# Optimization experiments

Hardware: AMD Instinct MI355X
Metric: run time of the kernel (lower is better)

The kernel has to match this reference:

```python
import jax, jax.numpy as jnp
import numpy as np

BATCH, IN_F, OUT_F = 4096, 1024, 1024


def setup_inputs() -> dict:
    key = jax.random.key(0)
    kx, kw = jax.random.split(key)
    x = jax.random.normal(kx, (BATCH, IN_F, 4), dtype=jnp.float32)
    weight = jax.random.normal(kw, (OUT_F, IN_F, 4), dtype=jnp.float32) * 0.01
    bias = jnp.zeros((OUT_F, 4), dtype=jnp.float32)
    return {"x": x, "weight": weight, "bias": bias}


def reference(x, weight, bias):
    # x: (batch, in, 4) quaternions; weight: (out, in, 4); bias: (out, 4)
    # Hamilton product broadcast over (batch, out, in) then summed over in ==
    # 16 signed real GEMMs contracting the `in` dimension.
    ar, ai, aj, ak = x[..., 0], x[..., 1], x[..., 2], x[..., 3]          # (b, i)
    br, bi, bj, bk = weight[..., 0], weight[..., 1], weight[..., 2], weight[..., 3]  # (o, i)

    mm = lambda a, w: jnp.einsum('bi,oi->bo', a, w)

    out_r = mm(ar, br) - mm(ai, bi) - mm(aj, bj) - mm(ak, bk)
    out_i = mm(ar, bi) + mm(ai, br) + mm(aj, bk) - mm(ak, bj)
    out_j = mm(ar, bj) - mm(ai, bk) + mm(aj, br) + mm(ak, bi)
    out_k = mm(ar, bk) + mm(ai, bj) - mm(aj, bi) + mm(ak, br)

    out = jnp.stack([out_r, out_i, out_j, out_k], axis=-1)  # (b, o, 4)
    return out + bias
```

## Files before the change

### kernel.cpp

```cpp
#include <hip/hip_runtime.h>


typedef __bf16 bf16x8 __attribute__((ext_vector_type(8)));
typedef float floatx4 __attribute__((ext_vector_type(4)));

constexpr int M = 4096;
constexpr int N = 4096;
constexpr int K = 4096;
constexpr int BM = 256, BN = 256, BK = 64;
constexpr int TILES = K / BK;

constexpr int CVT_BLOCKS = (M * K / 8) / 256;
constexpr int EXP_BLOCKS = (1024 * 1024 / 2) / 256;

#define WAIT_VM4 0x0F74
#define WAIT_VM0 0x0F70
#define BARRIER() asm volatile("s_barrier" ::: "memory")

__global__ void prep_kernel(const float* __restrict__ x, const float* __restrict__ w,
                            __bf16* __restrict__ A, __bf16* __restrict__ Wb) {
    const int b = blockIdx.x;
    if (b < CVT_BLOCKS) {
        const size_t i = (size_t)b * 256 + threadIdx.x;
        const float4* xp = (const float4*)x;
        float4 a = xp[2 * i];
        float4 c = xp[2 * i + 1];
        bf16x8 v;
        v[0] = (__bf16)a.x; v[1] = (__bf16)a.y; v[2] = (__bf16)a.z; v[3] = (__bf16)a.w;
        v[4] = (__bf16)c.x; v[5] = (__bf16)c.y; v[6] = (__bf16)c.z; v[7] = (__bf16)c.w;
        *(bf16x8*)(A + 8 * i) = v;
    } else {
        const int idx = (b - CVT_BLOCKS) * 256 + threadIdx.x;
        const int o  = idx >> 9;
        const int ip = (idx & 511) * 2;
        float4 q0 = ((const float4*)w)[o * 1024 + ip];
        float4 q1 = ((const float4*)w)[o * 1024 + ip + 1];
        __bf16* base = Wb + (size_t)(o * 4) * K + ip * 4;
        bf16x8 r;
        r[0] = (__bf16)q0.x; r[1] = (__bf16)(-q0.y); r[2] = (__bf16)(-q0.z); r[3] = (__bf16)(-q0.w);
        r[4] = (__bf16)q1.x; r[5] = (__bf16)(-q1.y); r[6] = (__bf16)(-q1.z); r[7] = (__bf16)(-q1.w);
        *(bf16x8*)(base) = r;
        r[0] = (__bf16)q0.y; r[1] = (__bf16)q0.x; r[2] = (__bf16)q0.w; r[3] = (__bf16)(-q0.z);
        r[4] = (__bf16)q1.y; r[5] = (__bf16)q1.x; r[6] = (__bf16)q1.w; r[7] = (__bf16)(-q1.z);
        *(bf16x8*)(base + (size_t)K) = r;
        r[0] = (__bf16)q0.z; r[1] = (__bf16)(-q0.w); r[2] = (__bf16)q0.x; r[3] = (__bf16)q0.y;
        r[4] = (__bf16)q1.z; r[5] = (__bf16)(-q1.w); r[6] = (__bf16)q1.x; r[7] = (__bf16)q1.y;
        *(bf16x8*)(base + (size_t)2 * K) = r;
        r[0] = (__bf16)q0.w; r[1] = (__bf16)q0.z; r[2] = (__bf16)(-q0.y); r[3] = (__bf16)q0.x;
        r[4] = (__bf16)q1.w; r[5] = (__bf16)q1.z; r[6] = (__bf16)(-q1.y); r[7] = (__bf16)q1.x;
        *(bf16x8*)(base + (size_t)3 * K) = r;
    }
}

__device__ __forceinline__ void gload_lds16(const __bf16* g, __bf16* l) {
    __builtin_amdgcn_global_load_lds(
        (const __attribute__((address_space(1))) void*)g,
        (__attribute__((address_space(3))) void*)l, 16, 0, 0);
}

__global__ __launch_bounds__(512) void qgemm_kernel(const __bf16* __restrict__ A,
                                                    const __bf16* __restrict__ B,
                                                    const float* __restrict__ bias,
                                                    float* __restrict__ C) {
    __shared__ __bf16 As[2][BM][BK];
    __shared__ __bf16 Bs[2][BN][BK];

    const int tid  = threadIdx.x;
    const int wave = tid >> 6;
    const int lane = tid & 63;

    const int bid = blockIdx.x;
    const int xcd = bid & 7;
    const int q   = bid >> 3;
    const int tm  = (xcd >> 2) * 8 + (q & 7);
    const int tn  = (xcd & 3) * 4 + (q >> 3);
    const int bm  = tm * BM;
    const int bn  = tn * BN;

    const int wm = (wave >> 2) * 128;
    const int wn = (wave & 3) * 64;

    const int srow = wave * 16 + (lane >> 3);
    const int schk = ((lane & 7) ^ (lane >> 3)) * 8;
    const __bf16* agA = A + (size_t)(bm + srow) * K + schk;
    const __bf16* agB = B + (size_t)(bn + srow) * K + schk;

    auto issueA = [&](int buf, int h, int t) {
        const __bf16* g = agA + (size_t)h * 128 * K + t * BK;
        gload_lds16(g,                 &As[buf][h * 128 + wave * 16][0]);
        gload_lds16(g + (size_t)8 * K, &As[buf][h * 128 + wave * 16 + 8][0]);
    };
    auto issueB = [&](int buf, int h, int t) {
        const __bf16* g = agB + (size_t)h * 128 * K + t * BK;
        gload_lds16(g,                 &Bs[buf][h * 128 + wave * 16][0]);
        gload_lds16(g + (size_t)8 * K, &Bs[buf][h * 128 + wave * 16 + 8][0]);
    };

    const int fl  = lane & 15;
    const int fq  = lane >> 4;
    const int fx7 = fl & 7;
    const int eo0 = (fq ^ fx7) * 8;
    const int eo1 = ((4 + fq) ^ fx7) * 8;

    floatx4 acc[8][4] = {};
    bf16x8 bF[4][2];

    issueA(0, 0, 0); issueA(0, 1, 0);
    issueB(0, 0, 0); issueB(0, 1, 0);
    issueB(1, 0, 1); issueB(1, 1, 1);
    __builtin_amdgcn_s_waitcnt(WAIT_VM4);
    BARRIER();

    for (int t = 0; t < TILES; ++t) {
        const int b = t & 1;
#pragma unroll
        for (int p = 0; p < 4; ++p) {
            bf16x8 aL0 = *(const bf16x8*)&As[b][wm + (2 * p) * 16 + fl][eo0];
            bf16x8 aL1 = *(const bf16x8*)&As[b][wm + (2 * p) * 16 + fl][eo1];
            bf16x8 aH0 = *(const bf16x8*)&As[b][wm + (2 * p + 1) * 16 + fl][eo0];
            bf16x8 aH1 = *(const bf16x8*)&As[b][wm + (2 * p + 1) * 16 + fl][eo1];
            if (p == 0) {
#pragma unroll
                for (int nt = 0; nt < 4; ++nt) {
                    bF[nt][0] = *(const bf16x8*)&Bs[b][wn + nt * 16 + fl][eo0];
                    bF[nt][1] = *(const bf16x8*)&Bs[b][wn + nt * 16 + fl][eo1];
                }
            }
            if (p == 0 && t + 1 < TILES) issueA(b ^ 1, 0, t + 1);
            if (p == 1 && t + 1 < TILES) issueA(b ^ 1, 1, t + 1);
            if (p == 2 && t + 2 < TILES) issueB(b, 0, t + 2);
            if (p == 3 && t + 2 < TILES) issueB(b, 1, t + 2);
            BARRIER();
            __builtin_amdgcn_s_setprio(1);
#pragma unroll
            for (int nt = 0; nt < 4; ++nt) {
                acc[2 * p][nt]     = __builtin_amdgcn_mfma_f32_16x16x32_bf16(
                    aL0, bF[nt][0], acc[2 * p][nt], 0, 0, 0);
                acc[2 * p + 1][nt] = __builtin_amdgcn_mfma_f32_16x16x32_bf16(
                    aH0, bF[nt][0], acc[2 * p + 1][nt], 0, 0, 0);
                acc[2 * p][nt]     = __builtin_amdgcn_mfma_f32_16x16x32_bf16(
                    aL1, bF[nt][1], acc[2 * p][nt], 0, 0, 0);
                acc[2 * p + 1][nt] = __builtin_amdgcn_mfma_f32_16x16x32_bf16(
                    aH1, bF[nt][1], acc[2 * p + 1][nt], 0, 0, 0);
            }
            __builtin_amdgcn_s_setprio(0);
            if (p == 3) {
                if (t + 2 < TILES) __builtin_amdgcn_s_waitcnt(WAIT_VM4);
                else               __builtin_amdgcn_s_waitcnt(WAIT_VM0);
            }
            BARRIER();
        }
    }

#pragma unroll
    for (int mt = 0; mt < 8; ++mt) {
        const int row = bm + wm + mt * 16 + fq * 4;
#pragma unroll
        for (int nt = 0; nt < 4; ++nt) {
            const int col = bn + wn + nt * 16 + fl;
            const float bv = bias[col];
            float* cp = C + (size_t)row * N + col;
#pragma unroll
            for (int r = 0; r < 4; ++r)
                cp[(size_t)r * N] = acc[mt][nt][r] + bv;
        }
    }
}

extern "C" void kernel_launch(void* const* d_in, const int* in_sizes, int n_in,
                              void* d_out, int out_size, void* d_ws, size_t ws_size,
                              hipStream_t stream) {
    const float* x    = (const float*)d_in[0];
    const float* w    = (const float*)d_in[1];
    const float* bias = (const float*)d_in[2];
    float* out = (float*)d_out;

    __bf16* Abf  = (__bf16*)d_ws;
    __bf16* Wbig = (__bf16*)((char*)d_ws + (size_t)M * K * 2);

    prep_kernel<<<CVT_BLOCKS + EXP_BLOCKS, 256, 0, stream>>>(x, w, Abf, Wbig);

    qgemm_kernel<<<256, 512, 0, stream>>>(Abf, Wbig, bias, out);
}
```

Baseline: 281.5 us.

## Use inline-asm LDS reads with explicit waits and reorder GEMM main loop

Replaces compiler-generated LDS loads with inline ds_read_b128 using precomputed byte offsets, and adds an explicit lgkmcnt(0) wait plus a sched_barrier before the MFMA block. Both A-tile prefetches are now issued in phase 0, the MFMA loop is split into two passes over the K halves, and launch_bounds asks for 2 blocks per CU. The aim is to control instruction scheduling and cut address arithmetic. In exchange, the compiler can no longer interleave LDS reads with MFMAs, which risks stalls. With 128KB of LDS per block, the second block per CU may not fit, so the launch_bounds change may only add register pressure.

```diff
diff --git a/kernel.cpp b/kernel.cpp
--- a/kernel.cpp
+++ b/kernel.cpp
@@ -13,9 +13,8 @@
 constexpr int CVT_BLOCKS = (M * K / 8) / 256;
 constexpr int EXP_BLOCKS = (1024 * 1024 / 2) / 256;
 
-#define WAIT_VM4 0x0F74
-#define WAIT_VM0 0x0F70
 #define BARRIER() asm volatile("s_barrier" ::: "memory")
+#define LDS_OFF(p) ((unsigned)(uintptr_t)(__attribute__((address_space(3))) const void*)(p))
 
 __global__ void prep_kernel(const float* __restrict__ x, const float* __restrict__ w,
                             __bf16* __restrict__ A, __bf16* __restrict__ Wb) {
@@ -58,10 +57,16 @@
         (__attribute__((address_space(3))) void*)l, 16, 0, 0);
 }
 
-__global__ __launch_bounds__(512) void qgemm_kernel(const __bf16* __restrict__ A,
-                                                    const __bf16* __restrict__ B,
-                                                    const float* __restrict__ bias,
-                                                    float* __restrict__ C) {
+__device__ __forceinline__ bf16x8 dsr128(unsigned addr) {
+    bf16x8 r;
+    asm volatile("ds_read_b128 %0, %1" : "=v"(r) : "v"(addr));
+    return r;
+}
+
+__global__ __launch_bounds__(512, 2) void qgemm_kernel(const __bf16* __restrict__ A,
+                                                       const __bf16* __restrict__ B,
+                                                       const float* __restrict__ bias,
+                                                       float* __restrict__ C) {
     __shared__ __bf16 As[2][BM][BK];
     __shared__ __bf16 Bs[2][BN][BK];
 
@@ -99,8 +104,10 @@
     const int fl  = lane & 15;
     const int fq  = lane >> 4;
     const int fx7 = fl & 7;
-    const int eo0 = (fq ^ fx7) * 8;
-    const int eo1 = ((4 + fq) ^ fx7) * 8;
+    const unsigned ebo0 = (unsigned)(((fq)     ^ fx7) * 16);
+    const unsigned ebo1 = (unsigned)(((4 + fq) ^ fx7) * 16);
+    const unsigned aRow = LDS_OFF(&As[0][0][0]) + (unsigned)(wm + fl) * 128u;
+    const unsigned bRow = LDS_OFF(&Bs[0][0][0]) + (unsigned)(wn + fl) * 128u;
 
     floatx4 acc[8][4] = {};
     bf16x8 bF[4][2];
@@ -108,29 +115,32 @@
     issueA(0, 0, 0); issueA(0, 1, 0);
     issueB(0, 0, 0); issueB(0, 1, 0);
     issueB(1, 0, 1); issueB(1, 1, 1);
-    __builtin_amdgcn_s_waitcnt(WAIT_VM4);
+    asm volatile("s_waitcnt vmcnt(4)");
     BARRIER();
 
     for (int t = 0; t < TILES; ++t) {
-        const int b = t & 1;
+        const int b  = t & 1;
+        const unsigned bs = (unsigned)b * 32768u;
 #pragma unroll
         for (int p = 0; p < 4; ++p) {
-            bf16x8 aL0 = *(const bf16x8*)&As[b][wm + (2 * p) * 16 + fl][eo0];
-            bf16x8 aL1 = *(const bf16x8*)&As[b][wm + (2 * p) * 16 + fl][eo1];
-            bf16x8 aH0 = *(const bf16x8*)&As[b][wm + (2 * p + 1) * 16 + fl][eo0];
-            bf16x8 aH1 = *(const bf16x8*)&As[b][wm + (2 * p + 1) * 16 + fl][eo1];
+            const unsigned pa = bs + (unsigned)(p * 4096);
+            bf16x8 aL0 = dsr128(aRow + pa + ebo0);
+            bf16x8 aL1 = dsr128(aRow + pa + ebo1);
+            bf16x8 aH0 = dsr128(aRow + pa + 2048u + ebo0);
+            bf16x8 aH1 = dsr128(aRow + pa + 2048u + ebo1);
             if (p == 0) {
 #pragma unroll
                 for (int nt = 0; nt < 4; ++nt) {
-                    bF[nt][0] = *(const bf16x8*)&Bs[b][wn + nt * 16 + fl][eo0];
-                    bF[nt][1] = *(const bf16x8*)&Bs[b][wn + nt * 16 + fl][eo1];
+                    bF[nt][0] = dsr128(bRow + bs + (unsigned)(nt * 2048) + ebo0);
+                    bF[nt][1] = dsr128(bRow + bs + (unsigned)(nt * 2048) + ebo1);
                 }
             }
-            if (p == 0 && t + 1 < TILES) issueA(b ^ 1, 0, t + 1);
-            if (p == 1 && t + 1 < TILES) issueA(b ^ 1, 1, t + 1);
+            if (p == 0 && t + 1 < TILES) { issueA(b ^ 1, 0, t + 1); issueA(b ^ 1, 1, t + 1); }
             if (p == 2 && t + 2 < TILES) issueB(b, 0, t + 2);
             if (p == 3 && t + 2 < TILES) issueB(b, 1, t + 2);
             BARRIER();
+            asm volatile("s_waitcnt lgkmcnt(0)");
+            __builtin_amdgcn_sched_barrier(0);
             __builtin_amdgcn_s_setprio(1);
 #pragma unroll
             for (int nt = 0; nt < 4; ++nt) {
@@ -138,6 +148,9 @@
                     aL0, bF[nt][0], acc[2 * p][nt], 0, 0, 0);
                 acc[2 * p + 1][nt] = __builtin_amdgcn_mfma_f32_16x16x32_bf16(
                     aH0, bF[nt][0], acc[2 * p + 1][nt], 0, 0, 0);
+            }
+#pragma unroll
+            for (int nt = 0; nt < 4; ++nt) {
                 acc[2 * p][nt]     = __builtin_amdgcn_mfma_f32_16x16x32_bf16(
                     aL1, bF[nt][1], acc[2 * p][nt], 0, 0, 0);
                 acc[2 * p + 1][nt] = __builtin_amdgcn_mfma_f32_16x16x32_bf16(
@@ -145,8 +158,8 @@
             }
             __builtin_amdgcn_s_setprio(0);
             if (p == 3) {
-                if (t + 2 < TILES) __builtin_amdgcn_s_waitcnt(WAIT_VM4);
-                else               __builtin_amdgcn_s_waitcnt(WAIT_VM0);
+                if (t + 2 < TILES) asm volatile("s_waitcnt vmcnt(4)");
+                else               asm volatile("s_waitcnt vmcnt(0)");
             }
             BARRIER();
         }
```

Measured after the change: 251.0 us. 1.12x faster.
